# Kernel optimization log

Hardware: AMD Instinct MI355X
Metric: run time of the kernel (lower is better)

The kernel has to match this reference:

```python
import jax, jax.numpy as jnp
import numpy as np

TEMP = 0.1


def _e8_roots() -> np.ndarray:
    # Type 1: (+-1, +-1, 0^6) in all coordinate pairs -> 112 roots
    r1 = []
    for i in range(8):
        for j in range(i + 1, 8):
            for si in (-1.0, 1.0):
                for sj in (-1.0, 1.0):
                    v = np.zeros(8, dtype=np.float32)
                    v[i] = si
                    v[j] = sj
                    r1.append(v)
    # Type 2: all +-0.5 with an even number of minus signs -> 128 roots
    r2 = []
    for mask in range(256):
        bits = [(mask >> b) & 1 for b in range(8)]
        if sum(bits) % 2 == 0:
            r2.append([-0.5 if b else 0.5 for b in bits])
    roots = np.concatenate([np.stack(r1), np.asarray(r2, dtype=np.float32)], axis=0)
    assert roots.shape == (240, 8)
    # Module applies F.normalize(p=2, dim=1) to the raw roots -> unit norm rows
    roots = roots / np.linalg.norm(roots, axis=1, keepdims=True)
    return roots.astype(np.float32)


def setup_inputs() -> dict:
    key = jax.random.key(0)
    x = jax.random.normal(key, (256, 4096, 8), dtype=jnp.float32)
    roots = jnp.asarray(_e8_roots())  # [240, 8], unit-norm
    return {"x": x, "roots": roots}


def reference(x, roots):
    x_norm_sq = jnp.sum(x * x, axis=-1, keepdims=True)      # [..., 1]
    roots_norm_sq = jnp.sum(roots * roots, axis=-1)          # [240]
    cross = jnp.einsum("btd,kd->btk", x, roots)             # [B, T, 240]
    distances = x_norm_sq - 2.0 * cross + roots_norm_sq      # [B, T, 240]
    weights = jax.nn.softmax(-distances / TEMP, axis=-1)     # [B, T, 240]
    quantized = jnp.einsum("btk,kd->btd", weights, roots)    # [B, T, 8]
    # Straight-through: value = quantized, gradient = identity w.r.t. x
    return x + jax.lax.stop_gradient(quantized - x)
```

## Files before the change

kernel.cpp:

```cpp
#include <hip/hip_runtime.h>
#include <math.h>

#define BLOCK 256

typedef float v4f __attribute__((ext_vector_type(4)));

struct EO { float E, O; };
__device__ __forceinline__ EO mergeEO(EO a, EO b) {
    EO r;
    r.E = fmaf(a.E, b.E, a.O * b.O);
    r.O = fmaf(a.E, b.O, a.O * b.E);
    return r;
}

__device__ __forceinline__ void e8q_token(const float xs[8], float o[8]) {
    float n2 = 0.0f;
#pragma unroll
    for (int j = 0; j < 8; ++j) n2 = fmaf(xs[j], xs[j], n2);
    const float xn = __builtin_amdgcn_sqrtf(n2);

    const float K2 = 10.201358186637847f;
    const float C  = 28.853900817779268f * xn;
    const float Ce = 0.125f * C;
    const float s  = __builtin_amdgcn_exp2f(-0.25f * C);

    float A[8], B[8], g[8], h[8];
#pragma unroll
    for (int j = 0; j < 8; ++j) {
        g[j] = __builtin_amdgcn_exp2f(fmaf(K2, xs[j], -Ce));
        h[j] = __builtin_amdgcn_exp2f(fmaf(-K2, xs[j], -Ce));
        float a = g[j] * g[j];
        float b = h[j] * h[j];
        float sa = s * a;
        A[j] = fmaf(s, b, sa);
        B[j] = fmaf(-s, b, sa);
    }

    float sufA[8];
    sufA[7] = A[7];
#pragma unroll
    for (int j = 6; j >= 0; --j) sufA[j] = sufA[j + 1] + A[j];

    float s1 = 0.0f;
#pragma unroll
    for (int j = 0; j < 7; ++j) s1 = fmaf(A[j], sufA[j + 1], s1);

    EO suf[8];
    suf[7] = {g[7], h[7]};
#pragma unroll
    for (int j = 6; j >= 1; --j) suf[j] = mergeEO({g[j], h[j]}, suf[j + 1]);

    const float s2 = mergeEO({g[0], h[0]}, suf[1]).E;

    const float inv = __builtin_amdgcn_rcpf(s1 + s2);
    const float c1 = 0.70710678118654752f * inv;
    const float c2 = 0.35355339059327376f * inv;

    float preA = 0.0f;
    EO preEO;
#pragma unroll
    for (int j = 0; j < 8; ++j) {
        float EA;
        EO ex;
        if (j == 0) {
            EA = sufA[1];
            ex = suf[1];
        } else if (j == 7) {
            EA = preA;
            ex = preEO;
        } else {
            EA = preA + sufA[j + 1];
            ex = mergeEO(preEO, suf[j + 1]);
        }
        float t2 = fmaf(g[j], ex.E, -(h[j] * ex.O));
        o[j] = fmaf(c1 * B[j], EA, c2 * t2);

        if (j == 0) {
            preA = A[0];
            preEO = {g[0], h[0]};
        } else {
            preA += A[j];
            preEO = mergeEO(preEO, {g[j], h[j]});
        }
    }
}

__global__ __launch_bounds__(BLOCK, 6) void e8q_kernel(const float* __restrict__ x,
                                                       float* __restrict__ out) {
    __shared__ v4f lA[BLOCK];
    __shared__ v4f lB[BLOCK];

    const int tid = threadIdx.x;
    const size_t tok0 = (size_t)blockIdx.x * BLOCK;

    const v4f* xp = (const v4f*)(x + (tok0 + tid) * 8);
    v4f a = xp[0];
    v4f b = xp[1];
    float xs[8] = {a.x, a.y, a.z, a.w, b.x, b.y, b.z, b.w};

    float o[8];
    e8q_token(xs, o);

    lA[tid] = (v4f){o[0], o[1], o[2], o[3]};
    lB[tid] = (v4f){o[4], o[5], o[6], o[7]};

    __syncthreads();

    v4f* outp = (v4f*)out + tok0 * 2;
#pragma unroll
    for (int k = 0; k < 2; ++k) {
        const int sidx = k * BLOCK + tid;
        v4f val = ((sidx & 1) ? lB : lA)[sidx >> 1];
        __builtin_nontemporal_store(val, outp + sidx);
    }
}

extern "C" void kernel_launch(void* const* d_in, const int* in_sizes, int n_in,
                              void* d_out, int out_size, void* d_ws, size_t ws_size,
                              hipStream_t stream) {
    const float* x = (const float*)d_in[0];
    float* out = (float*)d_out;

    const int tokens = in_sizes[0] / 8;
    const int grid = tokens / BLOCK;

    e8q_kernel<<<grid, BLOCK, 0, stream>>>(x, out);
}
```

Baseline: 14.92 us.

## Process two tokens per thread with wave-local LDS staging for coalesced I/O

Each 256-thread block now handles 512 tokens, two per thread. Each wave loads its input with contiguous, coalesced 16-byte accesses, transposes it through its own slice of shared memory, and writes results back the same way. Because the staging is wave-local, the block-wide barrier is gone. The cost is more registers and shared memory per thread, so the launch-bounds occupancy hint drops from 6 to 4. The kernel is close to memory-bound, so any gain likely comes from better load coalescing and more work in flight per thread.

```diff
diff --git a/kernel.cpp b/kernel.cpp
--- a/kernel.cpp
+++ b/kernel.cpp
@@ -2,6 +2,7 @@
 #include <math.h>
 
 #define BLOCK 256
+#define TPT 2
 
 typedef float v4f __attribute__((ext_vector_type(4)));
 
@@ -62,56 +63,63 @@
     for (int j = 0; j < 8; ++j) {
         float EA;
         EO ex;
-        if (j == 0) {
-            EA = sufA[1];
-            ex = suf[1];
-        } else if (j == 7) {
-            EA = preA;
-            ex = preEO;
-        } else {
-            EA = preA + sufA[j + 1];
-            ex = mergeEO(preEO, suf[j + 1]);
-        }
+        if (j == 0)      { EA = sufA[1];          ex = suf[1]; }
+        else if (j == 7) { EA = preA;             ex = preEO; }
+        else             { EA = preA + sufA[j+1]; ex = mergeEO(preEO, suf[j+1]); }
         float t2 = fmaf(g[j], ex.E, -(h[j] * ex.O));
         o[j] = fmaf(c1 * B[j], EA, c2 * t2);
-
-        if (j == 0) {
-            preA = A[0];
-            preEO = {g[0], h[0]};
-        } else {
-            preA += A[j];
-            preEO = mergeEO(preEO, {g[j], h[j]});
-        }
+        if (j == 0) { preA = A[0]; preEO = {g[0], h[0]}; }
+        else        { preA += A[j]; preEO = mergeEO(preEO, {g[j], h[j]}); }
     }
 }
 
-__global__ __launch_bounds__(BLOCK, 6) void e8q_kernel(const float* __restrict__ x,
+__global__ __launch_bounds__(BLOCK, 4) void e8q_kernel(const float* __restrict__ x,
                                                        float* __restrict__ out) {
-    __shared__ v4f lA[BLOCK];
-    __shared__ v4f lB[BLOCK];
+    __shared__ v4f inA[4][64 * TPT];
+    __shared__ v4f inB[4][64 * TPT];
+    __shared__ v4f outA[4][64 * TPT];
+    __shared__ v4f outB[4][64 * TPT];
 
     const int tid = threadIdx.x;
-    const size_t tok0 = (size_t)blockIdx.x * BLOCK;
+    const int w = tid >> 6;
+    const int l = tid & 63;
+    const size_t T0 = (size_t)blockIdx.x * (BLOCK * TPT);
+    const v4f* xv = (const v4f*)x + T0 * 2;
+    v4f* ov = (v4f*)out + T0 * 2;
 
-    const v4f* xp = (const v4f*)(x + (tok0 + tid) * 8);
-    v4f a = xp[0];
-    v4f b = xp[1];
-    float xs[8] = {a.x, a.y, a.z, a.w, b.x, b.y, b.z, b.w};
 
-    float o[8];
-    e8q_token(xs, o);
+    v4f ld[2 * TPT];
+#pragma unroll
+    for (int j = 0; j < 2; ++j) ld[j] = xv[128 * w + j * 64 + l];
+#pragma unroll
+    for (int j = 0; j < 2; ++j) ld[2 + j] = xv[512 + 128 * w + j * 64 + l];
 
-    lA[tid] = (v4f){o[0], o[1], o[2], o[3]};
-    lB[tid] = (v4f){o[4], o[5], o[6], o[7]};
+#pragma unroll
+    for (int j = 0; j < 2 * TPT; ++j) {
+        const int s = j * 64 + l;
+        if (s & 1) inB[w][s >> 1] = ld[j];
+        else       inA[w][s >> 1] = ld[j];
+    }
 
-    __syncthreads();
+#pragma unroll
+    for (int p = 0; p < TPT; ++p) {
+        const int tl = p * 64 + l;
+        v4f a = inA[w][tl];
+        v4f b = inB[w][tl];
+        float xs[8] = {a.x, a.y, a.z, a.w, b.x, b.y, b.z, b.w};
+        float o[8];
+        e8q_token(xs, o);
+        outA[w][tl] = (v4f){o[0], o[1], o[2], o[3]};
+        outB[w][tl] = (v4f){o[4], o[5], o[6], o[7]};
+    }
 
-    v4f* outp = (v4f*)out + tok0 * 2;
 #pragma unroll
-    for (int k = 0; k < 2; ++k) {
-        const int sidx = k * BLOCK + tid;
-        v4f val = ((sidx & 1) ? lB : lA)[sidx >> 1];
-        __builtin_nontemporal_store(val, outp + sidx);
+    for (int j = 0; j < 2 * TPT; ++j) {
+        const int s = j * 64 + l;
+        v4f val = (s & 1) ? outB[w][s >> 1] : outA[w][s >> 1];
+        const int gslot = (j < 2) ? (128 * w + j * 64 + l)
+                                  : (512 + 128 * w + (j - 2) * 64 + l);
+        __builtin_nontemporal_store(val, ov + gslot);
     }
 }
 
@@ -122,7 +130,7 @@
     float* out = (float*)d_out;
 
     const int tokens = in_sizes[0] / 8;
-    const int grid = tokens / BLOCK;
+    const int grid = tokens / (BLOCK * TPT);
 
     e8q_kernel<<<grid, BLOCK, 0, stream>>>(x, out);
 }
```

After: 15.52 us. 1.04x slower.
